# Kernel tuning notes

Measured on AMD Instinct MI355X. Metric: run time of the kernel, lower is better.

The kernel has to match this reference:

```python
import jax, jax.numpy as jnp
import numpy as np

N_CLUSTERS = 512
TEMPERATURE = 0.1


def setup_inputs() -> dict:
    key = jax.random.key(0)
    k1, k2 = jax.random.split(key)
    x = jax.random.normal(k1, (32, 1024, 256), dtype=jnp.float32)
    centroids = jax.random.normal(k2, (N_CLUSTERS, 256), dtype=jnp.float32)
    return {"x": x, "centroids": centroids}


def reference(x, centroids):
    # Flatten non-cluster axes into a sample axis: [N, D]
    B, S, D = x.shape
    xf = x.reshape(-1, D)  # [N, D]
    x_sq = jnp.sum(xf * xf, axis=-1, keepdims=True)           # [N, 1]
    c_sq = jnp.sum(centroids * centroids, axis=-1)             # [K]
    cross = jnp.einsum('nd,kd->nk', xf, centroids)             # [N, K]
    dists = x_sq - 2.0 * cross + c_sq[None, :]                 # [N, K]
    # Temperature-scaled soft assignments
    assignments = jax.nn.softmax(-dists / TEMPERATURE, axis=-1)  # [N, K]
    # Restore leading (non-feature) dims, append cluster axis
    return assignments.reshape(B, S, N_CLUSTERS)
```

## Files before the change

### kernel.cpp

```cpp
#include <hip/hip_runtime.h>

#define NROWS 32768
#define KC 512
#define DDIM 256
#define BM 128
#define BK 32
#define KCH (DDIM / BK)
#define CHUNK_USH (KC * BK)

typedef __attribute__((ext_vector_type(8))) short bf16x8;
typedef __attribute__((ext_vector_type(4))) float f32x4;

union U8 { unsigned short u[8]; bf16x8 v; };

__device__ __forceinline__ unsigned short f2bf(float f) {
    union { float f; unsigned int u; } a; a.f = f;
    unsigned int r = a.u + 0x7fffu + ((a.u >> 16) & 1u);
    return (unsigned short)(r >> 16);
}
__device__ __forceinline__ float bf2f(unsigned short h) {
    union { unsigned int u; float f; } a; a.u = ((unsigned int)h) << 16;
    return a.f;
}
__device__ __forceinline__ void ld16(const void* g, void* l) {
    __builtin_amdgcn_global_load_lds(
        (const __attribute__((address_space(1))) unsigned int*)g,
        (__attribute__((address_space(3))) unsigned int*)l, 16, 0, 0);
}

__global__ __launch_bounds__(64) void prep_c(const float* __restrict__ c,
                                             unsigned short* __restrict__ bhi,
                                             unsigned short* __restrict__ blo,
                                             float* __restrict__ csq10) {
    const int n = blockIdx.x, lane = threadIdx.x;
    const int d0 = lane * 4;
    float4 v = ((const float4*)(c + (size_t)n * DDIM))[lane];
    float vv[4] = {v.x, v.y, v.z, v.w};
    unsigned short hh[4], ll[4];
    float ssq = 0.f;
    #pragma unroll
    for (int i = 0; i < 4; ++i) {
        ssq += vv[i] * vv[i];
        hh[i] = f2bf(vv[i]);
        ll[i] = f2bf(vv[i] - bf2f(hh[i]));
    }
    #pragma unroll
    for (int off = 32; off; off >>= 1) ssq += __shfl_xor(ssq, off);
    if (lane == 0) csq10[n] = 10.f * ssq;
    const int ks = d0 >> 5;
    const int q  = (d0 >> 3) & 3;
    const int s  = q ^ ((n >> 1) & 3);
    const size_t dst = (size_t)ks * CHUNK_USH + (n * 4 + s) * 8 + (d0 & 7);
    *(ushort4*)(bhi + dst) = make_ushort4(hh[0], hh[1], hh[2], hh[3]);
    *(ushort4*)(blo + dst) = make_ushort4(ll[0], ll[1], ll[2], ll[3]);
}

union SmemU {
    struct { unsigned short Bh[2][CHUNK_USH], Bl[2][CHUNK_USH]; } k;
    float lbuf[32 * 516];
};

__global__ __launch_bounds__(512, 2) void kmeans_mfma(
    const float* __restrict__ x, const unsigned short* __restrict__ bhi,
    const unsigned short* __restrict__ blo, const float* __restrict__ csq10,
    float* __restrict__ out) {
    __shared__ __align__(16) SmemU sm;
    __shared__ float red[2][2][BM];

    const int tid  = threadIdx.x;
    const int w    = tid >> 6, lane = tid & 63;
    const int wm   = w >> 1, wn = w & 1;
    const int cc   = lane & 15, q = lane >> 4;
    const int row0 = blockIdx.x * BM;

    f32x4 acc[2][16];
    #pragma unroll
    for (int mt = 0; mt < 2; ++mt)
        #pragma unroll
        for (int t = 0; t < 16; ++t) acc[mt][t] = (f32x4){0.f, 0.f, 0.f, 0.f};

    const float* xA0 = x + (size_t)(row0 + wm * 32 + cc) * DDIM + q * 8;
    const float* xA1 = xA0 + (size_t)16 * DDIM;
    const int sF = q ^ ((cc >> 1) & 3);
    const int bF = (4 * cc + sF) * 8;
    const int dmaOff = (w * 4) * 512;

    float4 c00 = *(const float4*)xA0;
    float4 c01 = *(const float4*)(xA0 + 4);
    float4 c10 = *(const float4*)xA1;
    float4 c11 = *(const float4*)(xA1 + 4);
    #pragma unroll
    for (int j = 0; j < 4; ++j) {
        const int o = dmaOff + j * 512;
        ld16(bhi + o + lane * 8, &sm.k.Bh[0][o]);
        ld16(blo + o + lane * 8, &sm.k.Bl[0][o]);
    }

    #pragma unroll
    for (int ks = 0; ks < KCH; ++ks) {
        const int pp = ks & 1;
        bf16x8 ah[2], al[2];
        {
            float v0[8] = {c00.x, c00.y, c00.z, c00.w, c01.x, c01.y, c01.z, c01.w};
            float v1[8] = {c10.x, c10.y, c10.z, c10.w, c11.x, c11.y, c11.z, c11.w};
            U8 H0, L0, H1, L1;
            #pragma unroll
            for (int e = 0; e < 8; ++e) {
                H0.u[e] = f2bf(v0[e]); L0.u[e] = f2bf(v0[e] - bf2f(H0.u[e]));
                H1.u[e] = f2bf(v1[e]); L1.u[e] = f2bf(v1[e] - bf2f(H1.u[e]));
            }
            ah[0] = H0.v; al[0] = L0.v; ah[1] = H1.v; al[1] = L1.v;
        }
        float4 n00, n01, n10, n11;
        if (ks < KCH - 1) {
            const int kn = (ks + 1) * BK;
            n00 = *(const float4*)(xA0 + kn);
            n01 = *(const float4*)(xA0 + kn + 4);
            n10 = *(const float4*)(xA1 + kn);
            n11 = *(const float4*)(xA1 + kn + 4);
        }
        __builtin_amdgcn_sched_barrier(0);
        if (ks < KCH - 1) {
            asm volatile("s_waitcnt vmcnt(4)" ::: "memory");
        } else {
            asm volatile("s_waitcnt vmcnt(0)" ::: "memory");
        }
        __builtin_amdgcn_s_barrier();
        __builtin_amdgcn_sched_barrier(0);
        if (ks < KCH - 1) {
            const size_t cb = (size_t)(ks + 1) * CHUNK_USH;
            #pragma unroll
            for (int j = 0; j < 4; ++j) {
                const int o = dmaOff + j * 512;
                ld16(bhi + cb + o + lane * 8, &sm.k.Bh[1 - pp][o]);
                ld16(blo + cb + o + lane * 8, &sm.k.Bl[1 - pp][o]);
            }
        }
        #pragma unroll
        for (int grp = 0; grp < 4; ++grp) {
            bf16x8 bh[4], bl[4];
            #pragma unroll
            for (int tt = 0; tt < 4; ++tt) {
                const int bo = (wn * 16 + grp * 4 + tt) * 512 + bF;
                bh[tt] = *(const bf16x8*)&sm.k.Bh[pp][bo];
                bl[tt] = *(const bf16x8*)&sm.k.Bl[pp][bo];
            }
            #pragma unroll
            for (int tt = 0; tt < 4; ++tt) {
                const int t = grp * 4 + tt;
                acc[0][t] = __builtin_amdgcn_mfma_f32_16x16x32_bf16(ah[0], bh[tt], acc[0][t], 0, 0, 0);
                acc[1][t] = __builtin_amdgcn_mfma_f32_16x16x32_bf16(ah[1], bh[tt], acc[1][t], 0, 0, 0);
            }
            #pragma unroll
            for (int tt = 0; tt < 4; ++tt) {
                const int t = grp * 4 + tt;
                acc[0][t] = __builtin_amdgcn_mfma_f32_16x16x32_bf16(ah[0], bl[tt], acc[0][t], 0, 0, 0);
                acc[1][t] = __builtin_amdgcn_mfma_f32_16x16x32_bf16(ah[1], bl[tt], acc[1][t], 0, 0, 0);
            }
            #pragma unroll
            for (int tt = 0; tt < 4; ++tt) {
                const int t = grp * 4 + tt;
                acc[0][t] = __builtin_amdgcn_mfma_f32_16x16x32_bf16(al[0], bh[tt], acc[0][t], 0, 0, 0);
                acc[1][t] = __builtin_amdgcn_mfma_f32_16x16x32_bf16(al[1], bh[tt], acc[1][t], 0, 0, 0);
            }
        }
        c00 = n00; c01 = n01; c10 = n10; c11 = n11;
    }

    float csqv[16];
    #pragma unroll
    for (int t = 0; t < 16; ++t) csqv[t] = csq10[wn * 256 + t * 16 + cc];
    const int rb = wm * 32 + q * 4;
    float M[2][4], I[2][4];
    #pragma unroll
    for (int mt = 0; mt < 2; ++mt)
        #pragma unroll
        for (int g = 0; g < 4; ++g) {
            float pm = -1e30f;
            #pragma unroll
            for (int t = 0; t < 16; ++t) pm = fmaxf(pm, 20.f * acc[mt][t][g] - csqv[t]);
            #pragma unroll
            for (int off = 1; off < 16; off <<= 1) pm = fmaxf(pm, __shfl_xor(pm, off));
            if (cc == 0) red[0][wn][rb + mt * 16 + g] = pm;
            M[mt][g] = pm;
        }
    __syncthreads();
    #pragma unroll
    for (int mt = 0; mt < 2; ++mt)
        #pragma unroll
        for (int g = 0; g < 4; ++g) {
            M[mt][g] = fmaxf(M[mt][g], red[0][1 - wn][rb + mt * 16 + g]);
            float ps = 0.f;
            #pragma unroll
            for (int t = 0; t < 16; ++t) ps += __expf(20.f * acc[mt][t][g] - csqv[t] - M[mt][g]);
            #pragma unroll
            for (int off = 1; off < 16; off <<= 1) ps += __shfl_xor(ps, off);
            if (cc == 0) red[1][wn][rb + mt * 16 + g] = ps;
        }
    __syncthreads();
    #pragma unroll
    for (int mt = 0; mt < 2; ++mt)
        #pragma unroll
        for (int g = 0; g < 4; ++g)
            I[mt][g] = 1.f / (red[1][0][rb + mt * 16 + g] + red[1][1][rb + mt * 16 + g]);

    #pragma unroll
    for (int p = 0; p < 4; ++p) {
        if (wm == p) {
            #pragma unroll
            for (int mt = 0; mt < 2; ++mt)
                #pragma unroll
                for (int g = 0; g < 4; ++g) {
                    const int   lr = mt * 16 + q * 4 + g;
                    const float mg = M[mt][g], ig = I[mt][g];
                    #pragma unroll
                    for (int t = 0; t < 16; ++t)
                        sm.lbuf[lr * 516 + wn * 256 + t * 16 + cc] =
                            __expf(20.f * acc[mt][t][g] - csqv[t] - mg) * ig;
                }
        }
        __syncthreads();
        #pragma unroll
        for (int j = 0; j < 8; ++j) {
            const int f    = j * 512 + tid;
            const int lrow = f >> 7;
            const int c4   = f & 127;
            float4    v    = *(const float4*)&sm.lbuf[lrow * 516 + c4 * 4];
            *(float4*)(out + (size_t)(row0 + p * 32 + lrow) * KC + c4 * 4) = v;
        }
        __syncthreads();
    }
}

extern "C" void kernel_launch(void* const* d_in, const int* in_sizes, int n_in,
                              void* d_out, int out_size, void* d_ws, size_t ws_size,
                              hipStream_t stream) {
    const float* x   = (const float*)d_in[0];
    const float* c   = (const float*)d_in[1];
    float*       out = (float*)d_out;

    unsigned short* bhi   = (unsigned short*)d_ws;
    unsigned short* blo   = bhi + (size_t)KCH * CHUNK_USH;
    float*          csq10 = (float*)(blo + (size_t)KCH * CHUNK_USH);

    prep_c<<<KC, 64, 0, stream>>>(c, bhi, blo, csq10);
    kmeans_mfma<<<NROWS / BM, 512, 0, stream>>>(x, bhi, blo, csq10, out);
}
```

Before: 118.8 us.

## Double-buffer softmax epilogue staging and spread exp across all threads

The epilogue now stages raw logits (20*acc - csq) in two alternating 16-row LDS buffers. The exp/normalize work moves from the owning wave group to the threads doing the coalesced store, using per-row max and inverse-sum kept in shared arrays. Writing one 16-row slab overlaps with storing the previous one, so each phase needs one barrier instead of two. In exchange there are more barrier phases overall (9 instead of 4) and extra shared-memory reads of the row statistics.

```diff
diff --git a/kernel.cpp b/kernel.cpp
--- a/kernel.cpp
+++ b/kernel.cpp
@@ -57,7 +57,7 @@
 
 union SmemU {
     struct { unsigned short Bh[2][CHUNK_USH], Bl[2][CHUNK_USH]; } k;
-    float lbuf[32 * 516];
+    float lbuf[2][16 * 516];
 };
 
 __global__ __launch_bounds__(512, 2) void kmeans_mfma(
@@ -66,6 +66,7 @@
     float* __restrict__ out) {
     __shared__ __align__(16) SmemU sm;
     __shared__ float red[2][2][BM];
+    __shared__ float Mrow[BM], Irow[BM];
 
     const int tid  = threadIdx.x;
     const int w    = tid >> 6, lane = tid & 63;
@@ -201,32 +202,43 @@
     #pragma unroll
     for (int mt = 0; mt < 2; ++mt)
         #pragma unroll
-        for (int g = 0; g < 4; ++g)
+        for (int g = 0; g < 4; ++g) {
             I[mt][g] = 1.f / (red[1][0][rb + mt * 16 + g] + red[1][1][rb + mt * 16 + g]);
-
-    #pragma unroll
-    for (int p = 0; p < 4; ++p) {
-        if (wm == p) {
-            #pragma unroll
-            for (int mt = 0; mt < 2; ++mt)
+            if (wn == 0 && cc == 0) {
+                Mrow[rb + mt * 16 + g] = M[mt][g];
+                Irow[rb + mt * 16 + g] = I[mt][g];
+            }
+        }
+
+    #pragma unroll
+    for (int s = 0; s < 9; ++s) {
+        if (s < 8 && wm == (s >> 1)) {
+            const int mt = s & 1, b = s & 1;
+            #pragma unroll
+            for (int g = 0; g < 4; ++g)
                 #pragma unroll
-                for (int g = 0; g < 4; ++g) {
-                    const int   lr = mt * 16 + q * 4 + g;
-                    const float mg = M[mt][g], ig = I[mt][g];
-                    #pragma unroll
-                    for (int t = 0; t < 16; ++t)
-                        sm.lbuf[lr * 516 + wn * 256 + t * 16 + cc] =
-                            __expf(20.f * acc[mt][t][g] - csqv[t] - mg) * ig;
-                }
-        }
-        __syncthreads();
-        #pragma unroll
-        for (int j = 0; j < 8; ++j) {
-            const int f    = j * 512 + tid;
-            const int lrow = f >> 7;
-            const int c4   = f & 127;
-            float4    v    = *(const float4*)&sm.lbuf[lrow * 516 + c4 * 4];
-            *(float4*)(out + (size_t)(row0 + p * 32 + lrow) * KC + c4 * 4) = v;
+                for (int t = 0; t < 16; ++t)
+                    sm.lbuf[b][(q * 4 + g) * 516 + wn * 256 + t * 16 + cc] =
+                        fmaf(20.f, acc[mt][t][g], -csqv[t]);
+        }
+        if (s > 0) {
+            const int sp = s - 1, b2 = sp & 1;
+            const int rbase = (sp >> 1) * 32 + (sp & 1) * 16;
+            #pragma unroll
+            for (int j = 0; j < 4; ++j) {
+                const int f    = j * 512 + tid;
+                const int lrow = f >> 7;
+                const int c4   = f & 127;
+                float4 v = *(const float4*)&sm.lbuf[b2][lrow * 516 + c4 * 4];
+                const float m  = Mrow[rbase + lrow];
+                const float iv = Irow[rbase + lrow];
+                float4 o;
+                o.x = __expf(v.x - m) * iv;
+                o.y = __expf(v.y - m) * iv;
+                o.z = __expf(v.z - m) * iv;
+                o.w = __expf(v.w - m) * iv;
+                *(float4*)(out + (size_t)(row0 + rbase + lrow) * KC + c4 * 4) = o;
+            }
         }
         __syncthreads();
     }
```

After: 134.6 us. +13.3%, slower.

## Stage half of centroid tiles in LDS and read the rest from global

Applied to the files above, without the earlier changes.

Only half of each centroid chunk (tiles 0-7 and 16-23) is DMA-staged into shared memory, which halves the LDS footprint and the per-chunk copy traffic. The other half of the B fragments are loaded directly from global memory (expected to hit in L2) inside the MFMA loop. This may allow higher occupancy and less LDS bandwidth pressure, but it adds global-load latency on the critical path of the compute loop with no prefetch. The lbuf union member is unchanged, so the total shared-memory size may not actually shrink.

```diff
diff --git a/kernel.cpp b/kernel.cpp
--- a/kernel.cpp
+++ b/kernel.cpp
@@ -7,6 +7,7 @@
 #define BK 32
 #define KCH (DDIM / BK)
 #define CHUNK_USH (KC * BK)
+#define HALF_USH 8192
 
 typedef __attribute__((ext_vector_type(8))) short bf16x8;
 typedef __attribute__((ext_vector_type(4))) float f32x4;
@@ -56,7 +57,7 @@
 }
 
 union SmemU {
-    struct { unsigned short Bh[2][CHUNK_USH], Bl[2][CHUNK_USH]; } k;
+    struct { unsigned short Bh[2][HALF_USH], Bl[2][HALF_USH]; } k;
     float lbuf[32 * 516];
 };
 
@@ -83,18 +84,17 @@
     const float* xA1 = xA0 + (size_t)16 * DDIM;
     const int sF = q ^ ((cc >> 1) & 3);
     const int bF = (4 * cc + sF) * 8;
-    const int dmaOff = (w * 4) * 512;
+    const int st0 = w * 2;
+    const int T0  = (st0 < 8) ? st0 : st0 + 8;
 
     float4 c00 = *(const float4*)xA0;
     float4 c01 = *(const float4*)(xA0 + 4);
     float4 c10 = *(const float4*)xA1;
     float4 c11 = *(const float4*)(xA1 + 4);
-    #pragma unroll
-    for (int j = 0; j < 4; ++j) {
-        const int o = dmaOff + j * 512;
-        ld16(bhi + o + lane * 8, &sm.k.Bh[0][o]);
-        ld16(blo + o + lane * 8, &sm.k.Bl[0][o]);
-    }
+    ld16(bhi + (size_t)T0 * 512 + lane * 8,       &sm.k.Bh[0][st0 * 512]);
+    ld16(bhi + (size_t)(T0 + 1) * 512 + lane * 8, &sm.k.Bh[0][(st0 + 1) * 512]);
+    ld16(blo + (size_t)T0 * 512 + lane * 8,       &sm.k.Bl[0][st0 * 512]);
+    ld16(blo + (size_t)(T0 + 1) * 512 + lane * 8, &sm.k.Bl[0][(st0 + 1) * 512]);
 
     #pragma unroll
     for (int ks = 0; ks < KCH; ++ks) {
@@ -129,21 +129,29 @@
         __builtin_amdgcn_sched_barrier(0);
         if (ks < KCH - 1) {
             const size_t cb = (size_t)(ks + 1) * CHUNK_USH;
-            #pragma unroll
-            for (int j = 0; j < 4; ++j) {
-                const int o = dmaOff + j * 512;
-                ld16(bhi + cb + o + lane * 8, &sm.k.Bh[1 - pp][o]);
-                ld16(blo + cb + o + lane * 8, &sm.k.Bl[1 - pp][o]);
-            }
+            ld16(bhi + cb + T0 * 512 + lane * 8,       &sm.k.Bh[1 - pp][st0 * 512]);
+            ld16(bhi + cb + (T0 + 1) * 512 + lane * 8, &sm.k.Bh[1 - pp][(st0 + 1) * 512]);
+            ld16(blo + cb + T0 * 512 + lane * 8,       &sm.k.Bl[1 - pp][st0 * 512]);
+            ld16(blo + cb + (T0 + 1) * 512 + lane * 8, &sm.k.Bl[1 - pp][(st0 + 1) * 512]);
         }
         #pragma unroll
         for (int grp = 0; grp < 4; ++grp) {
             bf16x8 bh[4], bl[4];
-            #pragma unroll
-            for (int tt = 0; tt < 4; ++tt) {
-                const int bo = (wn * 16 + grp * 4 + tt) * 512 + bF;
-                bh[tt] = *(const bf16x8*)&sm.k.Bh[pp][bo];
-                bl[tt] = *(const bf16x8*)&sm.k.Bl[pp][bo];
+            if (grp < 2) {
+                #pragma unroll
+                for (int tt = 0; tt < 4; ++tt) {
+                    const int so = (wn * 8 + grp * 4 + tt) * 512 + bF;
+                    bh[tt] = *(const bf16x8*)&sm.k.Bh[pp][so];
+                    bl[tt] = *(const bf16x8*)&sm.k.Bl[pp][so];
+                }
+            } else {
+                const size_t go = (size_t)ks * CHUNK_USH + bF;
+                #pragma unroll
+                for (int tt = 0; tt < 4; ++tt) {
+                    const int T = wn * 16 + grp * 4 + tt;
+                    bh[tt] = *(const bf16x8*)(bhi + go + T * 512);
+                    bl[tt] = *(const bf16x8*)(blo + go + T * 512);
+                }
             }
             #pragma unroll
             for (int tt = 0; tt < 4; ++tt) {
```

After: 121.8 us. 2.5% more time.
